# Kernel tuning notes

Hardware: AMD Instinct MI355X
Metric: run time of the kernel (lower is better)

Reference implementation:

```python
import jax, jax.numpy as jnp
import numpy as np

B, NR, D_IN, D_CTX, H, A = 32, 4096, 384, 128, 64, 16
STD2 = 0.1
VAR2 = STD2 * STD2
LOG_VAR2 = float(np.log(VAR2))
TEMP = 1.0


def _l2norm(x, axis=-1):
    n = jnp.linalg.norm(x, axis=axis, keepdims=True)
    return x / jnp.maximum(n, 1e-12)


def _layernorm(x):
    # F.layer_norm over last dim, no affine, eps=1e-5, biased variance
    m = jnp.mean(x, axis=-1, keepdims=True)
    v = jnp.var(x, axis=-1, keepdims=True)
    return (x - m) / jnp.sqrt(v + 1e-5)


def setup_inputs() -> dict:
    key = jax.random.key(0)
    ks = jax.random.split(key, 16)
    def w(k, shape):
        return jax.random.normal(k, shape, jnp.float32) * 0.05
    return {
        "roles": jax.random.normal(ks[0], (B, NR, D_IN), jnp.float32),
        "contexts": jax.random.normal(ks[1], (B, D_CTX), jnp.float32),
        "eps": jax.random.normal(ks[2], (B, NR, H), jnp.float32),
        "rand_vals": jax.random.uniform(ks[3], (B, A), jnp.float32),
        "agent_num": A,
        "W1": w(ks[4], (D_IN, H)), "b1": jnp.zeros((H,), jnp.float32),
        "W21": w(ks[5], (H, H)), "b21": jnp.zeros((H,), jnp.float32),
        "W22": w(ks[6], (H, H)), "b22": jnp.zeros((H,), jnp.float32),
        "W3": w(ks[7], (H, H)), "b3": jnp.zeros((H,), jnp.float32),
        "W4": w(ks[8], (H, D_IN)), "b4": jnp.zeros((D_IN,), jnp.float32),
        "Wc": w(ks[9], (D_CTX + H, H)), "bc": jnp.zeros((H,), jnp.float32),
        "init_emb": jnp.zeros((H,), jnp.float32),
    }


def reference(roles, contexts, eps, rand_vals, agent_num,
              W1, b1, W21, b21, W22, b22, W3, b3, W4, b4, Wc, bc, init_emb):
    # --- VAE over all role pools at once: roles [B, NR, D_IN] ---
    h = jax.nn.relu(jnp.einsum('bnd,dh->bnh', roles, W1) + b1)       # [B,NR,H]
    mu = jnp.einsum('bnh,hk->bnk', h, W21) + b21                     # [B,NR,H]
    log_var = jnp.einsum('bnh,hk->bnk', h, W22) + b22                # [B,NR,H]
    z = mu + eps * (jnp.exp(0.5 * log_var) * STD2)                   # reparameterize
    x_hat = jnp.einsum('bnh,hd->bnd', jax.nn.relu(
        jnp.einsum('bnk,kh->bnh', z, W3) + b3), W4) + b4             # [B,NR,D_IN]
    role_emb = _l2norm(z, axis=-1)                                   # [B,NR,H]

    # vae_loss: per-item (mse mean + kld mean), summed over items, / B
    mse = jnp.mean((x_hat - roles) ** 2, axis=(1, 2))                # [B]
    kld = -0.5 * jnp.mean(
        1.0 - LOG_VAR2 + log_var - (mu ** 2 + jnp.exp(log_var)) / VAR2,
        axis=(1, 2))                                                 # [B]
    vae_loss = jnp.sum(mse + kld) / B

    # --- sequential role sampling per item (scan over agents, vmap over B) ---
    def per_item(emb, ctx_i, rands):
        # emb [NR,H], ctx_i [D_CTX], rands [A]
        def step(carry, r):
            hist, cur, lp = carry
            hist = _layernorm(hist + cur)                            # [H]
            c = jnp.concatenate([ctx_i, hist]) @ Wc + bc             # [H]
            c = c / jnp.maximum(jnp.linalg.norm(c), 1e-12)
            scores = jax.nn.softmax((emb @ c) / TEMP)                # [NR]
            sel = jnp.argmax(jnp.cumsum(scores) > r)                 # first True
            lp = lp + jnp.log(scores[sel])
            cur = emb[sel]
            return (hist, cur, lp), sel
        init = (init_emb, init_emb, jnp.zeros((), roles.dtype))
        (hist, _, lp), sels = jax.lax.scan(step, init, rands)
        return hist, lp, sels

    summary_role, log_p, sel_idx = jax.vmap(per_item)(role_emb, contexts, rand_vals)
    log_probs = log_p[:, None]                                       # [B,1]
    return sel_idx, log_probs, summary_role, vae_loss
```

## Files before the change

kernel.cpp:

```cpp
#include <hip/hip_runtime.h>
#include <math.h>

#define B_    32
#define NR_   4096
#define DIN_  384
#define DCTX_ 128
#define H__   64
#define A__   16
#define NROW_ (B_ * NR_)

#define WS_SUMS  0
#define WS_BAR   64
#define WS_SELW  6208
#define WS_SSC   8256
#define WS_SC0   10304
#define WS_ESUM  12352
#define WS_NSUM  45120
#define WS_EMBT  131072
#define WS_ZERO  12352

__device__ __forceinline__ float frelu(float x) { return fmaxf(x, 0.0f); }

struct alignas(16) Smem {
  union {
    struct { float As[32][68]; float Bs[32][68]; } p1;
    float zT[64][68];
    double red[256];
  } u;
  float hT[64][68];
  float rsq[16][66];
  float nrm[64];
};

__global__ __launch_bounds__(256, 4)
void vae_kernel(const float* __restrict__ roles,
                const float* __restrict__ eps,
                const float* __restrict__ W1,  const float* __restrict__ b1,
                const float* __restrict__ W21, const float* __restrict__ b21,
                const float* __restrict__ W22, const float* __restrict__ b22,
                const float* __restrict__ W3,  const float* __restrict__ b3,
                const float* __restrict__ W4,  const float* __restrict__ b4,
                float* __restrict__ embT, double* __restrict__ sums) {
  __shared__ Smem s;
  const int tid = threadIdx.x;
  const int tx = tid & 15, ty = tid >> 4;
  const int r0 = ty * 4, c0 = tx * 4;
  const long row_base = (long)blockIdx.x * 64;

  float acc[4][4];
#pragma unroll
  for (int i = 0; i < 4; i++)
#pragma unroll
    for (int j = 0; j < 4; j++) acc[i][j] = 0.0f;

  const int lr  = tid >> 2;
  const int lk0 = (tid & 3) * 8;
  const int bk  = tid >> 3;
  const int bc0 = (tid & 7) * 8;

  for (int ko = 0; ko < DIN_; ko += 32) {
    float4 a0 = *(const float4*)&roles[(row_base + lr) * DIN_ + ko + lk0];
    float4 a1 = *(const float4*)&roles[(row_base + lr) * DIN_ + ko + lk0 + 4];
    float4 w0 = *(const float4*)&W1[(ko + bk) * H__ + bc0];
    float4 w1 = *(const float4*)&W1[(ko + bk) * H__ + bc0 + 4];
    s.u.p1.As[lk0 + 0][lr] = a0.x; s.u.p1.As[lk0 + 1][lr] = a0.y;
    s.u.p1.As[lk0 + 2][lr] = a0.z; s.u.p1.As[lk0 + 3][lr] = a0.w;
    s.u.p1.As[lk0 + 4][lr] = a1.x; s.u.p1.As[lk0 + 5][lr] = a1.y;
    s.u.p1.As[lk0 + 6][lr] = a1.z; s.u.p1.As[lk0 + 7][lr] = a1.w;
    *(float4*)&s.u.p1.Bs[bk][bc0]     = w0;
    *(float4*)&s.u.p1.Bs[bk][bc0 + 4] = w1;
    __syncthreads();
#pragma unroll
    for (int kk = 0; kk < 32; kk++) {
      float4 av = *(const float4*)&s.u.p1.As[kk][r0];
      float4 bv = *(const float4*)&s.u.p1.Bs[kk][c0];
      float a_[4] = {av.x, av.y, av.z, av.w};
      float b_[4] = {bv.x, bv.y, bv.z, bv.w};
#pragma unroll
      for (int i = 0; i < 4; i++)
#pragma unroll
        for (int j = 0; j < 4; j++) acc[i][j] = fmaf(a_[i], b_[j], acc[i][j]);
    }
    __syncthreads();
  }
  {
    float4 bj = *(const float4*)&b1[c0];
    float bb[4] = {bj.x, bj.y, bj.z, bj.w};
#pragma unroll
    for (int j = 0; j < 4; j++)
#pragma unroll
      for (int i = 0; i < 4; i++)
        s.hT[c0 + j][r0 + i] = frelu(acc[i][j] + bb[j]);
  }
  __syncthreads();

  float mu[4][4], lv[4][4];
#pragma unroll
  for (int i = 0; i < 4; i++)
#pragma unroll
    for (int j = 0; j < 4; j++) { mu[i][j] = 0.0f; lv[i][j] = 0.0f; }
#pragma unroll 4
  for (int k = 0; k < 64; k++) {
    float4 hv  = *(const float4*)&s.hT[k][r0];
    float4 w21 = *(const float4*)&W21[k * H__ + c0];
    float4 w22 = *(const float4*)&W22[k * H__ + c0];
    float h_[4] = {hv.x, hv.y, hv.z, hv.w};
    float a_[4] = {w21.x, w21.y, w21.z, w21.w};
    float b_[4] = {w22.x, w22.y, w22.z, w22.w};
#pragma unroll
    for (int i = 0; i < 4; i++)
#pragma unroll
      for (int j = 0; j < 4; j++) {
        mu[i][j] = fmaf(h_[i], a_[j], mu[i][j]);
        lv[i][j] = fmaf(h_[i], b_[j], lv[i][j]);
      }
  }
  const float VAR2C = (float)0.010000000000000002;
  const float C1    = (float)5.605170185988091;
  double kacc = 0.0;
  float z[4][4];
  {
    float4 b21v = *(const float4*)&b21[c0];
    float4 b22v = *(const float4*)&b22[c0];
    float bb21[4] = {b21v.x, b21v.y, b21v.z, b21v.w};
    float bb22[4] = {b22v.x, b22v.y, b22v.z, b22v.w};
#pragma unroll
    for (int i = 0; i < 4; i++) {
      float4 ev = *(const float4*)&eps[(row_base + r0 + i) * H__ + c0];
      float e_[4] = {ev.x, ev.y, ev.z, ev.w};
#pragma unroll
      for (int j = 0; j < 4; j++) {
        float muv = mu[i][j] + bb21[j];
        float lvv = lv[i][j] + bb22[j];
        float zz  = muv + e_[j] * (expf(0.5f * lvv) * 0.1f);
        z[i][j] = zz;
        kacc += (double)((C1 + lvv) - (muv * muv + expf(lvv)) / VAR2C);
      }
    }
  }
#pragma unroll
  for (int i = 0; i < 4; i++) {
    float sq = 0.0f;
#pragma unroll
    for (int j = 0; j < 4; j++) {
      sq = fmaf(z[i][j], z[i][j], sq);
      s.u.zT[c0 + j][r0 + i] = z[i][j];
    }
    s.rsq[tx][r0 + i] = sq;
  }
  __syncthreads();
  if (tid < 64) {
    float t = 0.0f;
    for (int x = 0; x < 16; x++) t += s.rsq[x][tid];
    s.nrm[tid] = fmaxf(sqrtf(t), 1e-12f);
  }
  __syncthreads();

  {
    const int k  = tid >> 2;
    const int rs = (tid & 3) * 16;
#pragma unroll
    for (int q = 0; q < 4; q++) {
      float4 zv = *(const float4*)&s.u.zT[k][rs + 4 * q];
      float4 ov;
      ov.x = zv.x / s.nrm[rs + 4 * q + 0];
      ov.y = zv.y / s.nrm[rs + 4 * q + 1];
      ov.z = zv.z / s.nrm[rs + 4 * q + 2];
      ov.w = zv.w / s.nrm[rs + 4 * q + 3];
      *(float4*)&embT[(size_t)k * NROW_ + row_base + rs + 4 * q] = ov;
    }
  }

  float ta[4][4];
#pragma unroll
  for (int i = 0; i < 4; i++)
#pragma unroll
    for (int j = 0; j < 4; j++) ta[i][j] = 0.0f;
#pragma unroll 4
  for (int k = 0; k < 64; k++) {
    float4 zv = *(const float4*)&s.u.zT[k][r0];
    float4 wv = *(const float4*)&W3[k * H__ + c0];
    float z_[4] = {zv.x, zv.y, zv.z, zv.w};
    float w_[4] = {wv.x, wv.y, wv.z, wv.w};
#pragma unroll
    for (int i = 0; i < 4; i++)
#pragma unroll
      for (int j = 0; j < 4; j++) ta[i][j] = fmaf(z_[i], w_[j], ta[i][j]);
  }
  __syncthreads();
  {
    float4 b3v = *(const float4*)&b3[c0];
    float bb[4] = {b3v.x, b3v.y, b3v.z, b3v.w};
#pragma unroll
    for (int j = 0; j < 4; j++)
#pragma unroll
      for (int i = 0; i < 4; i++)
        s.hT[c0 + j][r0 + i] = frelu(ta[i][j] + bb[j]);
  }
  __syncthreads();

  double macc = 0.0;
  for (int dc = 0; dc < DIN_; dc += 64) {
    float xa[4][4];
#pragma unroll
    for (int i = 0; i < 4; i++)
#pragma unroll
      for (int j = 0; j < 4; j++) xa[i][j] = 0.0f;
#pragma unroll 4
    for (int k = 0; k < 64; k++) {
      float4 tv = *(const float4*)&s.hT[k][r0];
      float4 wv = *(const float4*)&W4[k * DIN_ + dc + c0];
      float t_[4] = {tv.x, tv.y, tv.z, tv.w};
      float w_[4] = {wv.x, wv.y, wv.z, wv.w};
#pragma unroll
      for (int i = 0; i < 4; i++)
#pragma unroll
        for (int j = 0; j < 4; j++) xa[i][j] = fmaf(t_[i], w_[j], xa[i][j]);
    }
    float4 b4v = *(const float4*)&b4[dc + c0];
    float bb[4] = {b4v.x, b4v.y, b4v.z, b4v.w};
#pragma unroll
    for (int i = 0; i < 4; i++) {
      float4 rv = *(const float4*)&roles[(row_base + r0 + i) * DIN_ + dc + c0];
      float r_[4] = {rv.x, rv.y, rv.z, rv.w};
#pragma unroll
      for (int j = 0; j < 4; j++) {
        float d = (xa[i][j] + bb[j]) - r_[j];
        macc += (double)(d * d);
      }
    }
  }

  __syncthreads();
  s.u.red[tid] = macc;
  __syncthreads();
  for (int st = 128; st > 0; st >>= 1) {
    if (tid < st) s.u.red[tid] += s.u.red[tid + st];
    __syncthreads();
  }
  if (tid == 0) atomicAdd(&sums[0], s.u.red[0]);
  __syncthreads();
  s.u.red[tid] = kacc;
  __syncthreads();
  for (int st = 128; st > 0; st >>= 1) {
    if (tid < st) s.u.red[tid] += s.u.red[tid + st];
    __syncthreads();
  }
  if (tid == 0) atomicAdd(&sums[1], s.u.red[0]);
}

__global__ void finalize_kernel(const double* __restrict__ sums,
                                float* __restrict__ out) {
  double mse_total = sums[0] / ((double)NR_ * (double)DIN_);
  double kld_total = -0.5 * (sums[1] / ((double)NR_ * (double)H__));
  out[512 + 32 + 2048] = (float)((mse_total + kld_total) / (double)B_);
}

__device__ __forceinline__ void batch_barrier(int* c) {
  __syncthreads();
  if (threadIdx.x == 0) {
    __hip_atomic_fetch_add(c, 1, __ATOMIC_ACQ_REL, __HIP_MEMORY_SCOPE_AGENT);
    while (__hip_atomic_load(c, __ATOMIC_ACQUIRE, __HIP_MEMORY_SCOPE_AGENT) < 8) {}
  }
  __syncthreads();
}

__global__ __launch_bounds__(256)
void select_kernel(const float* __restrict__ embT,
                   const float* __restrict__ contexts,
                   const float* __restrict__ rand_vals,
                   const float* __restrict__ Wc, const float* __restrict__ bc,
                   const float* __restrict__ init_emb,
                   char* __restrict__ ws,
                   float* __restrict__ out) {
  __shared__ float sEmb[64 * 512];
  __shared__ float sexp[512];
  __shared__ float hist[64], cur[64], cvec[64], ctxs[128];
  __shared__ float cpart[4][64];
  __shared__ double wtot[4];
  __shared__ int seli;

  int*    bar    = (int*)(ws + WS_BAR);
  int*    selw   = (int*)(ws + WS_SELW);
  float*  sscore = (float*)(ws + WS_SSC);
  float*  sc0    = (float*)(ws + WS_SC0);
  double* esum   = (double*)(ws + WS_ESUM);
  double* nsum   = (double*)(ws + WS_NSUM);

  const int tid   = threadIdx.x;
  const int slice = blockIdx.x >> 5;
  const int batch = blockIdx.x & 31;
  const int lane  = tid & 63, wid = tid >> 6;
  const size_t rowB  = (size_t)batch * NR_;
  const size_t base0 = rowB + (size_t)slice * 512;
  float lp = 0.0f;

  for (int i = tid; i < 64 * 128; i += 256) {
    const int k = i >> 7, j4 = (i & 127) << 2;
    *(float4*)&sEmb[k * 512 + j4] =
        *(const float4*)&embT[(size_t)k * NROW_ + base0 + j4];
  }
  if (tid < 64) { hist[tid] = init_emb[tid]; cur[tid] = init_emb[tid]; }
  if (tid < 128) ctxs[tid] = contexts[batch * DCTX_ + tid];
  __syncthreads();

  for (int step = 0; step < A__; step++) {
    const float  r  = rand_vals[batch * A__ + step];
    const double rd = (double)r;
    const int    bs = batch * A__ + step;

    if (tid < 64) {
      float v = hist[tid] + cur[tid];
      float sum = v;
      for (int o = 32; o > 0; o >>= 1) sum += __shfl_xor(sum, o);
      float m = sum / 64.0f;
      float d = v - m;
      float s2 = d * d;
      for (int o = 32; o > 0; o >>= 1) s2 += __shfl_xor(s2, o);
      hist[tid] = d / sqrtf(s2 / 64.0f + 1e-5f);
    }
    __syncthreads();
    {
      const int h = tid & 63, q = wid;
      float part = 0.0f;
      const int k0 = 48 * q;
#pragma unroll 8
      for (int k = k0; k < k0 + 48; k++) {
        float inv = (k < 128) ? ctxs[k] : hist[k - 128];
        part = fmaf(inv, Wc[k * H__ + h], part);
      }
      cpart[q][h] = part;
    }
    __syncthreads();
    if (tid < 64) {
      float a = bc[tid] + cpart[0][tid] + cpart[1][tid] + cpart[2][tid] + cpart[3][tid];
      float qq = a * a;
      for (int o = 32; o > 0; o >>= 1) qq += __shfl_xor(qq, o);
      cvec[tid] = a / fmaxf(sqrtf(qq), 1e-12f);
      if (tid == 0) seli = 0x7fffffff;
    }
    __syncthreads();
    float d0 = 0.0f, d1 = 0.0f;
    const float2* e2 = (const float2*)sEmb;
#pragma unroll 8
    for (int k = 0; k < 64; k++) {
      float2 ev = e2[k * 256 + tid];
      float c = cvec[k];
      d0 = fmaf(ev.x, c, d0);
      d1 = fmaf(ev.y, c, d1);
    }
    float e0 = expf(d0 - 1.0f), e1 = expf(d1 - 1.0f);
    double p = (double)e0 + (double)e1;
    double t = p;
    for (int o = 32; o > 0; o >>= 1) t += __shfl_xor(t, o);
    if (lane == 0) wtot[wid] = t;
    __syncthreads();
    if (tid == 0)
      esum[bs * 8 + slice] = ((wtot[0] + wtot[1]) + wtot[2]) + wtot[3];
    batch_barrier(&bar[(step * 3 + 0) * 32 + batch]);

    double denom = 0.0;
#pragma unroll
    for (int sx = 0; sx < 8; sx++) denom += esum[bs * 8 + sx];
    float s0 = (float)((double)e0 / denom);
    float s1 = (float)((double)e1 / denom);
    ((float2*)sexp)[tid] = make_float2(s0, s1);
    double p2 = (double)s0 + (double)s1;
    double ip = p2;
    for (int o = 1; o < 64; o <<= 1) {
      double u = __shfl_up(ip, o);
      if (lane >= o) ip += u;
    }
    __syncthreads();
    if (lane == 63) wtot[wid] = ip;
    __syncthreads();
    if (tid == 0)
      nsum[bs * 8 + slice] = ((wtot[0] + wtot[1]) + wtot[2]) + wtot[3];
    batch_barrier(&bar[(step * 3 + 1) * 32 + batch]);

    double base = 0.0;
    for (int sx = 0; sx < slice; sx++) base += nsum[bs * 8 + sx];
    double wbase = 0.0;
    for (int w = 0; w < wid; w++) wbase += wtot[w];
    double c = base + wbase + (ip - p2);
    int cand = 0x7fffffff;
    double cc = c + (double)s0;
    if (cc > rd) cand = 2 * tid;
    else { cc += (double)s1; if (cc > rd) cand = 2 * tid + 1; }
    if (cand != 0x7fffffff && rd >= base) atomicMin(&seli, cand);
    __syncthreads();
    if (tid == 0) {
      if (seli != 0x7fffffff && rd >= base) {
        selw[bs]   = slice * 512 + seli + 1;
        sscore[bs] = sexp[seli];
      }
      if (slice == 0) sc0[bs] = sexp[0];
    }
    batch_barrier(&bar[(step * 3 + 2) * 32 + batch]);

    const int sv  = selw[bs];
    const int sel = sv ? sv - 1 : 0;
    if (slice == 0 && tid == 0) {
      float sc = sv ? sscore[bs] : sc0[bs];
      lp += logf(sc);
      out[batch * A__ + step] = (float)sel;
    }
    if (tid < 64) cur[tid] = embT[(size_t)tid * NROW_ + rowB + sel];
    __syncthreads();
  }
  if (slice == 0 && tid == 0) out[512 + batch] = lp;
  if (slice == 0 && tid < 64) out[512 + 32 + batch * H__ + tid] = hist[tid];
}

extern "C" void kernel_launch(void* const* d_in, const int* in_sizes, int n_in,
                              void* d_out, int out_size, void* d_ws, size_t ws_size,
                              hipStream_t stream) {
  (void)in_sizes; (void)n_in; (void)out_size; (void)ws_size;
  const float* roles    = (const float*)d_in[0];
  const float* contexts = (const float*)d_in[1];
  const float* eps      = (const float*)d_in[2];
  const float* rand_v   = (const float*)d_in[3];
  const float* W1  = (const float*)d_in[5];
  const float* b1  = (const float*)d_in[6];
  const float* W21 = (const float*)d_in[7];
  const float* b21 = (const float*)d_in[8];
  const float* W22 = (const float*)d_in[9];
  const float* b22 = (const float*)d_in[10];
  const float* W3  = (const float*)d_in[11];
  const float* b3  = (const float*)d_in[12];
  const float* W4  = (const float*)d_in[13];
  const float* b4  = (const float*)d_in[14];
  const float* Wc  = (const float*)d_in[15];
  const float* bc  = (const float*)d_in[16];
  const float* iem = (const float*)d_in[17];
  float* out = (float*)d_out;

  char*   ws   = (char*)d_ws;
  double* sums = (double*)(ws + WS_SUMS);
  float*  embT = (float*)(ws + WS_EMBT);

  hipMemsetAsync(d_ws, 0, WS_ZERO, stream);
  vae_kernel<<<(B_ * NR_) / 64, 256, 0, stream>>>(
      roles, eps, W1, b1, W21, b21, W22, b22, W3, b3, W4, b4, embT, sums);
  finalize_kernel<<<1, 1, 0, stream>>>(sums, out);
  select_kernel<<<8 * B_, 256, 0, stream>>>(embT, contexts, rand_v, Wc, bc, iem,
                                            ws, out);
}
```

Baseline: 1.180 ms.

## Precompute context projection, cache hist weights in registers, publish selected embedding via workspace

After: 1.924 ms. 62.9% more time.

```diff
diff --git a/kernel.cpp b/kernel.cpp
--- a/kernel.cpp
+++ b/kernel.cpp
@@ -16,7 +16,9 @@
 #define WS_SC0   10304
 #define WS_ESUM  12352
 #define WS_NSUM  45120
-#define WS_EMBT  131072
+#define WS_CUR   77888
+#define WS_CUR0  208960
+#define WS_EMBT  340480
 #define WS_ZERO  12352
 
 __device__ __forceinline__ float frelu(float x) { return fmaxf(x, 0.0f); }
@@ -32,7 +34,7 @@
   float nrm[64];
 };
 
-__global__ __launch_bounds__(256, 4)
+__global__ __launch_bounds__(256) __attribute__((amdgpu_waves_per_eu(3)))
 void vae_kernel(const float* __restrict__ roles,
                 const float* __restrict__ eps,
                 const float* __restrict__ W1,  const float* __restrict__ b1,
@@ -99,7 +101,7 @@
   for (int i = 0; i < 4; i++)
 #pragma unroll
     for (int j = 0; j < 4; j++) { mu[i][j] = 0.0f; lv[i][j] = 0.0f; }
-#pragma unroll 4
+#pragma unroll 2
   for (int k = 0; k < 64; k++) {
     float4 hv  = *(const float4*)&s.hT[k][r0];
     float4 w21 = *(const float4*)&W21[k * H__ + c0];
@@ -257,12 +259,18 @@
 }
 
 __device__ __forceinline__ void batch_barrier(int* c) {
+  __threadfence();
   __syncthreads();
   if (threadIdx.x == 0) {
     __hip_atomic_fetch_add(c, 1, __ATOMIC_ACQ_REL, __HIP_MEMORY_SCOPE_AGENT);
     while (__hip_atomic_load(c, __ATOMIC_ACQUIRE, __HIP_MEMORY_SCOPE_AGENT) < 8) {}
   }
   __syncthreads();
+}
+
+template <typename T>
+__device__ __forceinline__ T aload(const T* p) {
+  return __hip_atomic_load(p, __ATOMIC_RELAXED, __HIP_MEMORY_SCOPE_AGENT);
 }
 
 __global__ __launch_bounds__(256)
@@ -277,6 +285,7 @@
   __shared__ float sexp[512];
   __shared__ float hist[64], cur[64], cvec[64], ctxs[128];
   __shared__ float cpart[4][64];
+  __shared__ float cconst[4][64];
   __shared__ double wtot[4];
   __shared__ int seli;
 
@@ -286,11 +295,14 @@
   float*  sc0    = (float*)(ws + WS_SC0);
   double* esum   = (double*)(ws + WS_ESUM);
   double* nsum   = (double*)(ws + WS_NSUM);
+  float*  curb   = (float*)(ws + WS_CUR);
+  float*  cur0b  = (float*)(ws + WS_CUR0);
 
   const int tid   = threadIdx.x;
   const int slice = blockIdx.x >> 5;
   const int batch = blockIdx.x & 31;
   const int lane  = tid & 63, wid = tid >> 6;
+  const int h = lane, q = wid;
   const size_t rowB  = (size_t)batch * NR_;
   const size_t base0 = rowB + (size_t)slice * 512;
   float lp = 0.0f;
@@ -302,6 +314,23 @@
   }
   if (tid < 64) { hist[tid] = init_emb[tid]; cur[tid] = init_emb[tid]; }
   if (tid < 128) ctxs[tid] = contexts[batch * DCTX_ + tid];
+  __syncthreads();
+
+  float wch[48];
+  if (q == 2) {
+#pragma unroll
+    for (int j = 0; j < 16; j++) wch[j] = Wc[(128 + j) * H__ + h];
+  } else if (q == 3) {
+#pragma unroll
+    for (int j = 0; j < 48; j++) wch[j] = Wc[(144 + j) * H__ + h];
+  }
+  {
+    float part = 0.0f;
+    const int k0 = 48 * q;
+    const int k1 = (k0 + 48 < 128) ? (k0 + 48) : 128;
+    for (int k = k0; k < k1; k++) part = fmaf(ctxs[k], Wc[k * H__ + h], part);
+    cconst[q][h] = part;
+  }
   __syncthreads();
 
   for (int step = 0; step < A__; step++) {
@@ -321,13 +350,13 @@
     }
     __syncthreads();
     {
-      const int h = tid & 63, q = wid;
-      float part = 0.0f;
-      const int k0 = 48 * q;
-#pragma unroll 8
-      for (int k = k0; k < k0 + 48; k++) {
-        float inv = (k < 128) ? ctxs[k] : hist[k - 128];
-        part = fmaf(inv, Wc[k * H__ + h], part);
+      float part = cconst[q][h];
+      if (q == 2) {
+#pragma unroll
+        for (int j = 0; j < 16; j++) part = fmaf(hist[j], wch[j], part);
+      } else if (q == 3) {
+#pragma unroll
+        for (int j = 0; j < 48; j++) part = fmaf(hist[16 + j], wch[j], part);
       }
       cpart[q][h] = part;
     }
@@ -361,7 +390,7 @@
 
     double denom = 0.0;
 #pragma unroll
-    for (int sx = 0; sx < 8; sx++) denom += esum[bs * 8 + sx];
+    for (int sx = 0; sx < 8; sx++) denom += aload(&esum[bs * 8 + sx]);
     float s0 = (float)((double)e0 / denom);
     float s1 = (float)((double)e1 / denom);
     ((float2*)sexp)[tid] = make_float2(s0, s1);
@@ -379,7 +408,7 @@
     batch_barrier(&bar[(step * 3 + 1) * 32 + batch]);
 
     double base = 0.0;
-    for (int sx = 0; sx < slice; sx++) base += nsum[bs * 8 + sx];
+    for (int sx = 0; sx < slice; sx++) base += aload(&nsum[bs * 8 + sx]);
     double wbase = 0.0;
     for (int w = 0; w < wid; w++) wbase += wtot[w];
     double c = base + wbase + (ip - p2);
@@ -389,23 +418,29 @@
     else { cc += (double)s1; if (cc > rd) cand = 2 * tid + 1; }
     if (cand != 0x7fffffff && rd >= base) atomicMin(&seli, cand);
     __syncthreads();
-    if (tid == 0) {
-      if (seli != 0x7fffffff && rd >= base) {
+    const bool is_owner = (seli != 0x7fffffff) && (rd >= base);
+    if (is_owner) {
+      if (tid == 0) {
         selw[bs]   = slice * 512 + seli + 1;
         sscore[bs] = sexp[seli];
       }
-      if (slice == 0) sc0[bs] = sexp[0];
+      if (tid < 64) curb[bs * 64 + tid] = sEmb[tid * 512 + seli];
+    }
+    if (slice == 0) {
+      if (tid == 0) sc0[bs] = sexp[0];
+      if (tid < 64) cur0b[bs * 64 + tid] = sEmb[tid * 512];
     }
     batch_barrier(&bar[(step * 3 + 2) * 32 + batch]);
 
-    const int sv  = selw[bs];
+    const int sv  = aload(&selw[bs]);
     const int sel = sv ? sv - 1 : 0;
     if (slice == 0 && tid == 0) {
-      float sc = sv ? sscore[bs] : sc0[bs];
+      float sc = sv ? aload(&sscore[bs]) : aload(&sc0[bs]);
       lp += logf(sc);
       out[batch * A__ + step] = (float)sel;
     }
-    if (tid < 64) cur[tid] = embT[(size_t)tid * NROW_ + rowB + sel];
+    if (tid < 64)
+      cur[tid] = sv ? aload(&curb[bs * 64 + tid]) : aload(&cur0b[bs * 64 + tid]);
     __syncthreads();
   }
   if (slice == 0 && tid == 0) out[512 + batch] = lp;
```
